# Kernel tuning notes

Hardware: AMD Instinct MI355X
Metric: run time of the kernel (lower is better)

The kernel has to match this reference:

```python
import jax, jax.numpy as jnp
import numpy as np

TOP_K = 2
NORM_TOPK_PROB = True


def setup_inputs() -> dict:
    key = jax.random.key(0)
    k1, k2, k3 = jax.random.split(key, 3)
    B, S, H, E = 4, 2048, 2048, 8
    hidden_states = jax.random.normal(k1, (B, S, H), dtype=jnp.float32)
    gate_w = jax.random.normal(k2, (E, H), dtype=jnp.float32) * 0.02   # nn.Linear weight [E, H]
    expert_w = jax.random.normal(k3, (E, H, H), dtype=jnp.float32) * 0.02  # per-expert Linear weight [H_out, H_in]
    return {"hidden_states": hidden_states, "gate_w": gate_w, "expert_w": expert_w}


def reference(hidden_states, gate_w, expert_w):
    B, S, H = hidden_states.shape
    E = gate_w.shape[0]
    x = hidden_states.reshape(-1, H)                      # [T, H], T = B*S
    T = x.shape[0]

    router_logits = x @ gate_w.T                          # [T, E]
    probs = jax.nn.softmax(router_logits.astype(jnp.float32), axis=-1)
    top_w, top_i = jax.lax.top_k(probs, TOP_K)            # [T, K]
    if NORM_TOPK_PROB:
        top_w = top_w / jnp.sum(top_w, axis=-1, keepdims=True)
    top_w = top_w.astype(x.dtype)

    # dense [T, E] combine weights (scatter of top-k weights)
    w_full = jnp.zeros((T, E), dtype=x.dtype).at[jnp.arange(T)[:, None], top_i].add(top_w)

    # expert_i(x) = x @ W_i.T  (bias-free Linear)
    expert_out = jnp.einsum('th,eoh->eto', x, expert_w)   # [E, T, H]
    out = jnp.einsum('te,eto->to', w_full, expert_out)    # [T, H]

    return out.reshape(B, S, H), router_logits.reshape(B, S, E)
```

## Files before the change

kernel.cpp:

```cpp
#include <hip/hip_runtime.h>
#include <stdint.h>

#define T_TOK 8192
#define HDIM  2048
#define NEXP  8
#define TILE  128
#define BK    64
#define RTOK  32

typedef __bf16 bf16x8 __attribute__((ext_vector_type(8)));
typedef float  f32x4  __attribute__((ext_vector_type(4)));
typedef unsigned short u16;
typedef u16    u16x8  __attribute__((ext_vector_type(8)));

typedef const __attribute__((address_space(1))) void* gptr_t;
typedef __attribute__((address_space(3))) void* lptr_t;

static __device__ __forceinline__ u16 f2bf(float f) {
    union { float f; unsigned u; } v; v.f = f;
    unsigned u = v.u;
    u = (u + 0x7FFFu + ((u >> 16) & 1u)) >> 16;
    return (u16)u;
}

__global__ __launch_bounds__(256) void cvt_kernel(const float* __restrict__ in,
                                                  u16* __restrict__ out, int n8) {
    int i = blockIdx.x * 256 + threadIdx.x;
    if (i >= n8) return;
    const float4* p = (const float4*)in + (size_t)i * 2;
    float4 a = p[0], b = p[1];
    u16x8 r;
    r[0] = f2bf(a.x); r[1] = f2bf(a.y); r[2] = f2bf(a.z); r[3] = f2bf(a.w);
    r[4] = f2bf(b.x); r[5] = f2bf(b.y); r[6] = f2bf(b.z); r[7] = f2bf(b.w);
    ((u16x8*)out)[i] = r;
}

__global__ __launch_bounds__(256) void router_kernel(const float* __restrict__ x,
                                                     const float* __restrict__ gw,
                                                     u16* __restrict__ xb,
                                                     float* __restrict__ logits_out,
                                                     int* __restrict__ cnt,
                                                     int* __restrict__ rows,
                                                     float* __restrict__ wts) {
    __shared__ int   lcnt[NEXP];
    __shared__ int   lbase[NEXP];
    __shared__ int   lrows[NEXP][RTOK];
    __shared__ float lwtsS[NEXP][RTOK];

    int tid  = threadIdx.x;
    int lane = tid & 63;
    int wave = tid >> 6;
    if (tid < NEXP) lcnt[tid] = 0;
    __syncthreads();

    int t0 = blockIdx.x * RTOK + wave * 8;
    const float4* g4 = (const float4*)gw;

    float acc[8][NEXP] = {};
    #pragma unroll
    for (int i = 0; i < HDIM / 4 / 64; i++) {
        int idx = lane + i * 64;
        float4 gv[NEXP];
        #pragma unroll
        for (int e = 0; e < NEXP; e++) gv[e] = g4[e * (HDIM / 4) + idx];
        #pragma unroll
        for (int tk = 0; tk < 8; tk++) {
            int t = t0 + tk;
            float4 xv = ((const float4*)(x + (size_t)t * HDIM))[idx];
            ushort4 h;
            h.x = f2bf(xv.x); h.y = f2bf(xv.y); h.z = f2bf(xv.z); h.w = f2bf(xv.w);
            ((ushort4*)(xb + (size_t)t * HDIM))[idx] = h;
            #pragma unroll
            for (int e = 0; e < NEXP; e++)
                acc[tk][e] += xv.x * gv[e].x + xv.y * gv[e].y +
                              xv.z * gv[e].z + xv.w * gv[e].w;
        }
    }
    #pragma unroll
    for (int tk = 0; tk < 8; tk++)
        #pragma unroll
        for (int e = 0; e < NEXP; e++)
            #pragma unroll
            for (int off = 32; off > 0; off >>= 1)
                acc[tk][e] += __shfl_xor(acc[tk][e], off, 64);

    if (lane == 0) {
        #pragma unroll
        for (int tk = 0; tk < 8; tk++) {
            int t = t0 + tk;
            #pragma unroll
            for (int e = 0; e < NEXP; e++) logits_out[(size_t)t * NEXP + e] = acc[tk][e];
            int e0 = 0;
            #pragma unroll
            for (int e = 1; e < NEXP; e++) if (acc[tk][e] > acc[tk][e0]) e0 = e;
            int e1 = (e0 == 0) ? 1 : 0;
            #pragma unroll
            for (int e = 0; e < NEXP; e++)
                if (e != e0 && acc[tk][e] > acc[tk][e1]) e1 = e;
            float w0 = 1.0f / (1.0f + expf(acc[tk][e1] - acc[tk][e0]));
            int p0 = atomicAdd(&lcnt[e0], 1);
            lrows[e0][p0] = t; lwtsS[e0][p0] = w0;
            int p1 = atomicAdd(&lcnt[e1], 1);
            lrows[e1][p1] = t; lwtsS[e1][p1] = 1.0f - w0;
        }
    }
    __syncthreads();
    if (tid < NEXP) lbase[tid] = atomicAdd(&cnt[tid], lcnt[tid]);
    __syncthreads();
    int e = tid >> 5, j = tid & 31;
    if (j < lcnt[e]) {
        int b = lbase[e] + j;
        rows[e * T_TOK + b] = lrows[e][j];
        wts[e * T_TOK + b]  = lwtsS[e][j];
    }
}

__global__ __launch_bounds__(256) void moe_gemm(const u16* __restrict__ xb,
                                                const u16* __restrict__ wb,
                                                const int* __restrict__ cnt,
                                                const int* __restrict__ rows,
                                                const float* __restrict__ wts,
                                                float* __restrict__ out) {
    int p  = blockIdx.x;
    int xc = p & 7;
    int q  = p >> 3;
    int rt = q & 63;
    int g  = (q >> 6) * 8 + xc;
    int e  = g >> 4;
    int nb = (g & 15) * TILE;

    int count = cnt[e];
    int rowBase = rt * TILE;
    if (rowBase >= count) return;

    const u16*   W     = wb  + (size_t)e * HDIM * HDIM;
    const int*   rlist = rows + e * T_TOK;
    const float* wlist = wts  + e * T_TOK;

    __shared__ u16 As[TILE * BK];
    __shared__ u16 Bs[TILE * BK];

    int tid  = threadIdx.x;
    int lane = tid & 63;
    int wave = tid >> 6;
    int wr = wave >> 1, wc = wave & 1;

    const u16* a_src[4];
    const u16* b_src[4];
    #pragma unroll
    for (int pp = 0; pp < 4; pp++) {
        int row  = (tid >> 3) + pp * 32;
        int clog = (tid & 7) ^ (row & 7);
        int tok  = rlist[min(rowBase + row, count - 1)];
        a_src[pp] = xb + (size_t)tok * HDIM + clog * 8;
        b_src[pp] = W + (size_t)(nb + row) * HDIM + clog * 8;
    }
    int wslot = (tid & ~63);
    u16* lds_a[4]; u16* lds_b[4];
    #pragma unroll
    for (int pp = 0; pp < 4; pp++) {
        lds_a[pp] = As + (size_t)(pp * 256 + wslot) * 8;
        lds_b[pp] = Bs + (size_t)(pp * 256 + wslot) * 8;
    }

    int lrow = lane & 15;
    int kq   = lane >> 4;
    int mloc[4], nloc[4];
    #pragma unroll
    for (int i = 0; i < 4; i++) {
        mloc[i] = wr * 64 + i * 16 + lrow;
        nloc[i] = wc * 64 + i * 16 + lrow;
    }

    f32x4 acc[4][4] = {};

    for (int kb = 0; kb < HDIM; kb += BK) {
        __syncthreads();
        #pragma unroll
        for (int pp = 0; pp < 4; pp++) {
            __builtin_amdgcn_global_load_lds((gptr_t)(a_src[pp] + kb),
                                             (lptr_t)lds_a[pp], 16, 0, 0);
            __builtin_amdgcn_global_load_lds((gptr_t)(b_src[pp] + kb),
                                             (lptr_t)lds_b[pp], 16, 0, 0);
        }
        __syncthreads();

        #pragma unroll
        for (int s = 0; s < 2; s++) {
            int chunk = s * 4 + kq;
            bf16x8 a[4], b[4];
            #pragma unroll
            for (int i = 0; i < 4; i++) {
                int aslot = (mloc[i] << 3) | (chunk ^ (mloc[i] & 7));
                int bslot = (nloc[i] << 3) | (chunk ^ (nloc[i] & 7));
                a[i] = *(const bf16x8*)(As + aslot * 8);
                b[i] = *(const bf16x8*)(Bs + bslot * 8);
            }
            #pragma unroll
            for (int mt = 0; mt < 4; mt++)
                #pragma unroll
                for (int nt = 0; nt < 4; nt++)
                    acc[mt][nt] = __builtin_amdgcn_mfma_f32_16x16x32_bf16(
                                      a[mt], b[nt], acc[mt][nt], 0, 0, 0);
        }
    }

    int srow = (lane >> 4) * 4;
    #pragma unroll
    for (int mt = 0; mt < 4; mt++) {
        #pragma unroll
        for (int r = 0; r < 4; r++) {
            int row = rowBase + wr * 64 + mt * 16 + srow + r;
            if (row < count) {
                int   tok = rlist[row];
                float wgt = wlist[row];
                #pragma unroll
                for (int nt = 0; nt < 4; nt++) {
                    int col = nb + wc * 64 + nt * 16 + lrow;
                    atomicAdd(out + (size_t)tok * HDIM + col, wgt * acc[mt][nt][r]);
                }
            }
        }
    }
}

extern "C" void kernel_launch(void* const* d_in, const int* in_sizes, int n_in,
                              void* d_out, int out_size, void* d_ws, size_t ws_size,
                              hipStream_t stream) {
    const float* x  = (const float*)d_in[0];
    const float* gw = (const float*)d_in[1];
    const float* ew = (const float*)d_in[2];
    float* out    = (float*)d_out;
    float* logits = out + (size_t)T_TOK * HDIM;

    char* ws = (char*)d_ws;
    int*   cnt  = (int*)ws;
    int*   rows = (int*)(ws + 1024);
    float* wts  = (float*)(ws + 1024 + 262144);
    u16*   xb   = (u16*)(ws + 1024 + 2 * 262144);
    u16*   wb   = xb + (size_t)T_TOK * HDIM;

    hipMemsetAsync(d_out, 0, (size_t)T_TOK * HDIM * sizeof(float), stream);
    hipMemsetAsync(cnt, 0, NEXP * sizeof(int), stream);

    int nw8 = NEXP * HDIM * HDIM / 8;
    cvt_kernel<<<(nw8 + 255) / 256, 256, 0, stream>>>(ew, wb, nw8);

    router_kernel<<<T_TOK / RTOK, 256, 0, stream>>>(x, gw, xb, logits, cnt, rows, wts);

    moe_gemm<<<NEXP * 64 * 16, 256, 0, stream>>>(xb, wb, cnt, rows, wts, out);
}
```

Before: 644.1 us.

## Pack routed token rows per expert into contiguous padded bf16 buffer before GEMM

Instead of converting all activations to bf16 in the router and gathering rows by token index inside the GEMM, a new setup kernel computes padded per-expert offsets. A pack kernel then gathers, converts and zero-pads each expert's tokens into a contiguous buffer. The GEMM now loads A tiles from contiguous rows rather than scattered token rows, which should improve coalescing and cache behaviour. The cost is two extra kernel launches and a separate gather pass that reads x a second time, and the routing rows now encode the top-k slot in their low bit.

```diff
diff --git a/kernel.cpp b/kernel.cpp
--- a/kernel.cpp
+++ b/kernel.cpp
@@ -7,6 +7,7 @@
 #define TILE  128
 #define BK    64
 #define RTOK  32
+#define PADGRID 17408
 
 typedef __bf16 bf16x8 __attribute__((ext_vector_type(8)));
 typedef float  f32x4  __attribute__((ext_vector_type(4)));
@@ -37,7 +38,6 @@
 
 __global__ __launch_bounds__(256) void router_kernel(const float* __restrict__ x,
                                                      const float* __restrict__ gw,
-                                                     u16* __restrict__ xb,
                                                      float* __restrict__ logits_out,
                                                      int* __restrict__ cnt,
                                                      int* __restrict__ rows,
@@ -67,9 +67,6 @@
         for (int tk = 0; tk < 8; tk++) {
             int t = t0 + tk;
             float4 xv = ((const float4*)(x + (size_t)t * HDIM))[idx];
-            ushort4 h;
-            h.x = f2bf(xv.x); h.y = f2bf(xv.y); h.z = f2bf(xv.z); h.w = f2bf(xv.w);
-            ((ushort4*)(xb + (size_t)t * HDIM))[idx] = h;
             #pragma unroll
             for (int e = 0; e < NEXP; e++)
                 acc[tk][e] += xv.x * gv[e].x + xv.y * gv[e].y +
@@ -99,9 +96,9 @@
                 if (e != e0 && acc[tk][e] > acc[tk][e1]) e1 = e;
             float w0 = 1.0f / (1.0f + expf(acc[tk][e1] - acc[tk][e0]));
             int p0 = atomicAdd(&lcnt[e0], 1);
-            lrows[e0][p0] = t; lwtsS[e0][p0] = w0;
+            lrows[e0][p0] = t * 2;     lwtsS[e0][p0] = w0;
             int p1 = atomicAdd(&lcnt[e1], 1);
-            lrows[e1][p1] = t; lwtsS[e1][p1] = 1.0f - w0;
+            lrows[e1][p1] = t * 2 + 1; lwtsS[e1][p1] = 1.0f - w0;
         }
     }
     __syncthreads();
@@ -115,9 +112,48 @@
     }
 }
 
-__global__ __launch_bounds__(256) void moe_gemm(const u16* __restrict__ xb,
+__global__ void setup_kernel(const int* __restrict__ cnt, int* __restrict__ ebase) {
+    if (threadIdx.x == 0 && blockIdx.x == 0) {
+        int s = 0;
+        for (int e = 0; e < NEXP; e++) {
+            ebase[e] = s;
+            s += (cnt[e] + TILE - 1) & ~(TILE - 1);
+        }
+        ebase[NEXP] = s;
+    }
+}
+
+__global__ __launch_bounds__(256) void pack_kernel(const float* __restrict__ x,
+                                                   const int* __restrict__ cnt,
+                                                   const int* __restrict__ ebase,
+                                                   const int* __restrict__ rows,
+                                                   u16* __restrict__ Xg) {
+    int j = blockIdx.x;
+    if (j >= ebase[NEXP]) return;
+    int e = 0;
+    #pragma unroll
+    for (int k = 1; k < NEXP; k++) if (j >= ebase[k]) e = k;
+    int r = j - ebase[e];
+    u16x8* dst = (u16x8*)(Xg + (size_t)j * HDIM) + threadIdx.x;
+    if (r < cnt[e]) {
+        int tok = rows[e * T_TOK + r] >> 1;
+        const float4* p = (const float4*)(x + (size_t)tok * HDIM) +
+                          (size_t)threadIdx.x * 2;
+        float4 a = p[0], b = p[1];
+        u16x8 v;
+        v[0] = f2bf(a.x); v[1] = f2bf(a.y); v[2] = f2bf(a.z); v[3] = f2bf(a.w);
+        v[4] = f2bf(b.x); v[5] = f2bf(b.y); v[6] = f2bf(b.z); v[7] = f2bf(b.w);
+        *dst = v;
+    } else {
+        u16x8 z = {};
+        *dst = z;
+    }
+}
+
+__global__ __launch_bounds__(256) void moe_gemm(const u16* __restrict__ Xg,
                                                 const u16* __restrict__ wb,
                                                 const int* __restrict__ cnt,
+                                                const int* __restrict__ ebase,
                                                 const int* __restrict__ rows,
                                                 const float* __restrict__ wts,
                                                 float* __restrict__ out) {
@@ -136,6 +172,7 @@
     const u16*   W     = wb  + (size_t)e * HDIM * HDIM;
     const int*   rlist = rows + e * T_TOK;
     const float* wlist = wts  + e * T_TOK;
+    const u16*   Abase = Xg + (size_t)(ebase[e] + rowBase) * HDIM;
 
     __shared__ u16 As[TILE * BK];
     __shared__ u16 Bs[TILE * BK];
@@ -151,8 +188,7 @@
     for (int pp = 0; pp < 4; pp++) {
         int row  = (tid >> 3) + pp * 32;
         int clog = (tid & 7) ^ (row & 7);
-        int tok  = rlist[min(rowBase + row, count - 1)];
-        a_src[pp] = xb + (size_t)tok * HDIM + clog * 8;
+        a_src[pp] = Abase + (size_t)row * HDIM + clog * 8;
         b_src[pp] = W + (size_t)(nb + row) * HDIM + clog * 8;
     }
     int wslot = (tid & ~63);
@@ -212,7 +248,7 @@
         for (int r = 0; r < 4; r++) {
             int row = rowBase + wr * 64 + mt * 16 + srow + r;
             if (row < count) {
-                int   tok = rlist[row];
+                int   tok = rlist[row] >> 1;
                 float wgt = wlist[row];
                 #pragma unroll
                 for (int nt = 0; nt < 4; nt++) {
@@ -234,11 +270,12 @@
     float* logits = out + (size_t)T_TOK * HDIM;
 
     char* ws = (char*)d_ws;
-    int*   cnt  = (int*)ws;
-    int*   rows = (int*)(ws + 1024);
-    float* wts  = (float*)(ws + 1024 + 262144);
-    u16*   xb   = (u16*)(ws + 1024 + 2 * 262144);
-    u16*   wb   = xb + (size_t)T_TOK * HDIM;
+    int*   cnt   = (int*)ws;
+    int*   ebase = (int*)(ws + 128);
+    int*   rows  = (int*)(ws + 1024);
+    float* wts   = (float*)(ws + 1024 + 262144);
+    u16*   wb    = (u16*)(ws + (1 << 20));
+    u16*   Xg    = wb + (size_t)NEXP * HDIM * HDIM;
 
     hipMemsetAsync(d_out, 0, (size_t)T_TOK * HDIM * sizeof(float), stream);
     hipMemsetAsync(cnt, 0, NEXP * sizeof(int), stream);
@@ -246,7 +283,11 @@
     int nw8 = NEXP * HDIM * HDIM / 8;
     cvt_kernel<<<(nw8 + 255) / 256, 256, 0, stream>>>(ew, wb, nw8);
 
-    router_kernel<<<T_TOK / RTOK, 256, 0, stream>>>(x, gw, xb, logits, cnt, rows, wts);
-
-    moe_gemm<<<NEXP * 64 * 16, 256, 0, stream>>>(xb, wb, cnt, rows, wts, out);
-}
+    router_kernel<<<T_TOK / RTOK, 256, 0, stream>>>(x, gw, logits, cnt, rows, wts);
+
+    setup_kernel<<<1, 64, 0, stream>>>(cnt, ebase);
+
+    pack_kernel<<<PADGRID, 256, 0, stream>>>(x, cnt, ebase, rows, Xg);
+
+    moe_gemm<<<NEXP * 64 * 16, 256, 0, stream>>>(Xg, wb, cnt, ebase, rows, wts, out);
+}
```

Result: no change. 645.3 us (+0.2%).
